# Kernel tuning notes

Hardware: AMD Instinct MI355X
Metric: run time of the kernel (lower is better)

## Reference

```python
import jax, jax.numpy as jnp
import numpy as np

B, S, H, KV, D, HID = 1, 2048, 32, 8, 128, 4096
SCALE = D ** -0.5
EPS = 1e-5
QMAX = 127.0  # 8-bit symmetric fake quant


def fake_quant(x):
    # per-tensor symmetric int8 fake quantization with straight-through estimator
    s = jnp.maximum(jnp.max(jnp.abs(x)), 1e-5) / QMAX
    q = jnp.clip(jnp.round(x / s), -QMAX - 1.0, QMAX) * s
    return x + jax.lax.stop_gradient(q - x)


def rms_norm(x, w):
    xf = x.astype(jnp.float32)
    var = jnp.mean(xf * xf, axis=-1, keepdims=True)
    return (xf * jax.lax.rsqrt(var + EPS)).astype(x.dtype) * w


def rotate_half(x):
    h = x.shape[-1] // 2
    return jnp.concatenate([-x[..., h:], x[..., :h]], axis=-1)


def qlinear(x, W):
    # QuantLinear: fake-quant activation and weight, then matmul (no bias)
    return fake_quant(x) @ fake_quant(W).T


def setup_inputs() -> dict:
    key = jax.random.key(0)
    ks = jax.random.split(key, 5)
    hidden_states = jax.random.normal(ks[0], (B, S, HID), jnp.float32)
    # RoPE tables
    inv_freq = 1.0 / (10000.0 ** (np.arange(0, D, 2, dtype=np.float32) / D))
    freqs = np.outer(np.arange(S, dtype=np.float32), inv_freq)  # [S, D/2]
    emb = np.concatenate([freqs, freqs], axis=-1)  # [S, D]
    cos = jnp.asarray(np.cos(emb))[None]  # [1,S,D]
    sin = jnp.asarray(np.sin(emb))[None]
    # causal additive mask [1,1,S,S]
    mask = jnp.where(np.tril(np.ones((S, S), dtype=bool)), 0.0, -1e9).astype(jnp.float32)[None, None]
    Wq = jax.random.normal(ks[1], (H * D, HID), jnp.float32) * 0.02
    Wk = jax.random.normal(ks[2], (KV * D, HID), jnp.float32) * 0.02
    Wv = jax.random.normal(ks[3], (KV * D, HID), jnp.float32) * 0.02
    Wo = jax.random.normal(ks[4], (HID, H * D), jnp.float32) * 0.02
    q_norm_w = jnp.ones((D,), jnp.float32)
    k_norm_w = jnp.ones((D,), jnp.float32)
    return dict(hidden_states=hidden_states, cos=cos, sin=sin, attention_mask=mask,
                Wq=Wq, Wk=Wk, Wv=Wv, Wo=Wo, q_norm_w=q_norm_w, k_norm_w=k_norm_w)


def reference(hidden_states, cos, sin, attention_mask, Wq, Wk, Wv, Wo, q_norm_w, k_norm_w):
    b, s, _ = hidden_states.shape
    q = qlinear(hidden_states, Wq).reshape(b, s, H, D).transpose(0, 2, 1, 3)   # [B,H,S,D]
    k = qlinear(hidden_states, Wk).reshape(b, s, KV, D).transpose(0, 2, 1, 3)  # [B,KV,S,D]
    v = qlinear(hidden_states, Wv).reshape(b, s, KV, D).transpose(0, 2, 1, 3)
    q = rms_norm(q, q_norm_w)
    k = rms_norm(k, k_norm_w)
    c = cos[:, None]  # unsqueeze head dim -> [1,1,S,D]
    sn = sin[:, None]
    q = q * c + rotate_half(q) * sn
    k = k * c + rotate_half(k) * sn
    n_rep = H // KV
    k = jnp.repeat(k, n_rep, axis=1)  # [B,H,S,D]
    v = jnp.repeat(v, n_rep, axis=1)
    # fake-quant around QK^T
    q = fake_quant(q)
    k = fake_quant(k)
    scores = jnp.einsum('bhqd,bhkd->bhqk', q, k) * SCALE + attention_mask
    p = jax.nn.softmax(scores.astype(jnp.float32), axis=-1).astype(q.dtype)
    # fake-quant around PV
    p = fake_quant(p)
    v = fake_quant(v)
    out = jnp.einsum('bhqk,bhkd->bhqd', p, v)
    out = out.transpose(0, 2, 1, 3).reshape(b, s, H * D)
    return qlinear(out, Wo)
```

## Files before the change

kernel.cpp:

```cpp
#include <hip/hip_runtime.h>
#include <hip/hip_bf16.h>
#include <math.h>
#include <stdint.h>

#define S_LEN 2048
#define NH    32
#define NKV   8
#define HD    128
#define HIDD  4096

typedef unsigned short u16;
typedef __attribute__((ext_vector_type(4))) int i32x4;

#define GLD16(g, l) __builtin_amdgcn_global_load_lds( \
    (const __attribute__((address_space(1))) void*)(g), \
    (__attribute__((address_space(3))) void*)(l), 16, 0, 0)


__device__ __forceinline__ float slot_scale(const unsigned* slot) {
    return fmaxf(__uint_as_float(*slot), 1e-5f) / 127.0f;
}

__device__ __forceinline__ float exp2_fast(float x) {
    float r; asm("v_exp_f32 %0, %1" : "=v"(r) : "v"(x)); return r;
}
__device__ __forceinline__ float log2_fast(float x) {
    float r; asm("v_log_f32 %0, %1" : "=v"(r) : "v"(x)); return r;
}

__device__ __forceinline__ int qint(float x, float s) {
    float q = rintf(x / s);
    q = fminf(fmaxf(q, -128.0f), 127.0f);
    return (int)q;
}

__device__ __forceinline__ void block_amax_atomic(float m, unsigned* slot) {
    __shared__ float wmax[8];
    const int lane = threadIdx.x & 63;
    const int wid  = threadIdx.x >> 6;
    const int nw   = blockDim.x >> 6;
    #pragma unroll
    for (int o = 32; o; o >>= 1) m = fmaxf(m, __shfl_xor(m, o));
    if (lane == 0) wmax[wid] = m;
    __syncthreads();
    if (threadIdx.x == 0) {
        float bm = wmax[0];
        for (int i = 1; i < nw; ++i) bm = fmaxf(bm, wmax[i]);
        atomicMax(slot, __float_as_uint(bm));
    }
}

struct Amax5Args { const float* p[5]; size_t n4[5]; };
__global__ __launch_bounds__(256) void absmax5_kernel(Amax5Args a, unsigned* slots) {
    const int t = blockIdx.y;
    const float4* x4 = (const float4*)a.p[t];
    const size_t n4 = a.n4[t];
    size_t i = (size_t)blockIdx.x * blockDim.x + threadIdx.x;
    size_t stride = (size_t)gridDim.x * blockDim.x;
    float m = 0.0f;
    for (; i < n4; i += stride) {
        float4 v = x4[i];
        m = fmaxf(m, fmaxf(fmaxf(fabsf(v.x), fabsf(v.y)), fmaxf(fabsf(v.z), fabsf(v.w))));
    }
    block_amax_atomic(m, slots + t);
}

struct Quant5Args { const float* p[5]; char* o[5]; size_t n4[5]; };
__global__ __launch_bounds__(256) void quant5_kernel(Quant5Args a, const unsigned* slots) {
    const int t = blockIdx.y;
    float s = slot_scale(slots + t);
    const float4* x4 = (const float4*)a.p[t];
    unsigned* o4 = (unsigned*)a.o[t];
    const size_t n4 = a.n4[t];
    size_t i = (size_t)blockIdx.x * blockDim.x + threadIdx.x;
    size_t stride = (size_t)gridDim.x * blockDim.x;
    for (; i < n4; i += stride) {
        float4 v = x4[i];
        unsigned o = (unsigned)(qint(v.x, s) & 255)
                   | ((unsigned)(qint(v.y, s) & 255) << 8)
                   | ((unsigned)(qint(v.z, s) & 255) << 16)
                   | ((unsigned)(qint(v.w, s) & 255) << 24);
        o4[i] = o;
    }
}

__global__ __launch_bounds__(256) void quant_kernel(const float* __restrict__ x,
                                                    size_t n4, const unsigned* slot,
                                                    char* __restrict__ out) {
    float s = slot_scale(slot);
    size_t i = (size_t)blockIdx.x * blockDim.x + threadIdx.x;
    size_t stride = (size_t)gridDim.x * blockDim.x;
    const float4* x4 = (const float4*)x;
    unsigned* o4 = (unsigned*)out;
    for (; i < n4; i += stride) {
        float4 v = x4[i];
        unsigned o = (unsigned)(qint(v.x, s) & 255)
                   | ((unsigned)(qint(v.y, s) & 255) << 8)
                   | ((unsigned)(qint(v.z, s) & 255) << 16)
                   | ((unsigned)(qint(v.w, s) & 255) << 24);
        o4[i] = o;
    }
}

__device__ __forceinline__ void gemm_body(const char* __restrict__ A,
                                          const char* __restrict__ B,
                                          float* __restrict__ C,
                                          int m0, int n0, int N, int K,
                                          float scale, unsigned* out_amax,
                                          char* Asm, char* Bsm) {
    const int tid  = threadIdx.x;
    const int lane = tid & 63;
    const int wave = tid >> 6;
    const int wr = (wave >> 1) * 64;
    const int wc = (wave & 1) * 64;
    const int l15 = lane & 15;
    const int l4  = lane >> 4;
    const int cx  = (l4 ^ (l15 & 3)) * 16;
    const int r0  = tid >> 2;
    const int sc  = ((tid & 3) ^ ((tid >> 2) & 3)) * 16;

    i32x4 acc[4][4];
    #pragma unroll
    for (int i = 0; i < 4; ++i)
        #pragma unroll
        for (int j = 0; j < 4; ++j) acc[i][j] = (i32x4){0, 0, 0, 0};

    auto STAGE = [&](int buf, int k0) {
        GLD16(&A[(size_t)(m0 + r0) * K + k0 + sc],      &Asm[buf * 8192 + wave * 1024]);
        GLD16(&A[(size_t)(m0 + 64 + r0) * K + k0 + sc], &Asm[buf * 8192 + 4096 + wave * 1024]);
        GLD16(&B[(size_t)(n0 + r0) * K + k0 + sc],      &Bsm[buf * 8192 + wave * 1024]);
        GLD16(&B[(size_t)(n0 + 64 + r0) * K + k0 + sc], &Bsm[buf * 8192 + 4096 + wave * 1024]);
    };

    const int NT = K >> 6;
    STAGE(0, 0);
    STAGE(1, 64);
    int cur = 0;
    for (int t = 0; t < NT; ++t) {
        if (t + 1 < NT) {
            asm volatile("s_waitcnt vmcnt(4)" ::: "memory");
        } else {
            asm volatile("s_waitcnt vmcnt(0)" ::: "memory");
        }
        __builtin_amdgcn_sched_barrier(0);
        __builtin_amdgcn_s_barrier();
        __builtin_amdgcn_sched_barrier(0);
        if (t + 2 < NT) {
            int nb = cur + 2; if (nb >= 3) nb -= 3;
            STAGE(nb, (t + 2) << 6);
        }
        i32x4 af[4], bfr[4];
        #pragma unroll
        for (int i = 0; i < 4; ++i)
            af[i] = *(const i32x4*)&Asm[cur * 8192 + (wr + i * 16 + l15) * 64 + cx];
        #pragma unroll
        for (int j = 0; j < 4; ++j)
            bfr[j] = *(const i32x4*)&Bsm[cur * 8192 + (wc + j * 16 + l15) * 64 + cx];
        #pragma unroll
        for (int i = 0; i < 4; ++i)
            #pragma unroll
            for (int j = 0; j < 4; ++j)
                acc[i][j] = __builtin_amdgcn_mfma_i32_16x16x64_i8(af[i], bfr[j], acc[i][j], 0, 0, 0);
        cur += 1; if (cur == 3) cur = 0;
    }

    float lm = 0.0f;
    #pragma unroll
    for (int i = 0; i < 4; ++i)
        #pragma unroll
        for (int j = 0; j < 4; ++j)
            #pragma unroll
            for (int r = 0; r < 4; ++r) {
                int row = m0 + wr + i * 16 + l4 * 4 + r;
                int col = n0 + wc + j * 16 + l15;
                float v = (float)acc[i][j][r] * scale;
                C[(size_t)row * N + col] = v;
                lm = fmaxf(lm, fabsf(v));
            }
    __syncthreads();
    if (out_amax) block_amax_atomic(lm, out_amax);
}

__global__ __launch_bounds__(256) void gemm_qkv_kernel(const char* __restrict__ Aq,
                                                       const char* __restrict__ Wqq,
                                                       const char* __restrict__ Wkq,
                                                       const char* __restrict__ Wvq,
                                                       float* __restrict__ qf,
                                                       float* __restrict__ kf,
                                                       float* __restrict__ vf,
                                                       const unsigned* __restrict__ slots,
                                                       unsigned* v_amax) {
    __shared__ __align__(16) char Asm[3 * 8192];
    __shared__ __align__(16) char Bsm[3 * 8192];
    int bid = blockIdx.x;
    int swz = (bid & 7) * 96 + (bid >> 3);
    int x = swz & 15, y = swz >> 4;
    const char* B; float* C; int N, nb; const unsigned* sB; unsigned* am = nullptr;
    if (y < 32)      { B = Wqq; C = qf; N = NH * HD;  nb = y;      sB = slots + 1; }
    else if (y < 40) { B = Wkq; C = kf; N = NKV * HD; nb = y - 32; sB = slots + 2; }
    else             { B = Wvq; C = vf; N = NKV * HD; nb = y - 40; sB = slots + 3; am = v_amax; }
    float scale = slot_scale(slots + 0) * slot_scale(sB);
    gemm_body(Aq, B, C, x * 128, nb * 128, N, HIDD, scale, am, Asm, Bsm);
}

__global__ __launch_bounds__(256) void gemm_o_kernel(const char* __restrict__ A,
                                                     const char* __restrict__ Woq,
                                                     float* __restrict__ C,
                                                     const unsigned* __restrict__ slots) {
    __shared__ __align__(16) char Asm[3 * 8192];
    __shared__ __align__(16) char Bsm[3 * 8192];
    int bid = blockIdx.x;
    int swz = (bid & 7) * 64 + (bid >> 3);
    int x = swz & 15, y = swz >> 4;
    float scale = slot_scale(slots + 8) * slot_scale(slots + 4);
    gemm_body(A, Woq, C, x * 128, y * 128, NH * HD, HIDD, scale, nullptr, Asm, Bsm);
}

__global__ __launch_bounds__(256) void rmsrope2_kernel(float* __restrict__ qx,
                                                       float* __restrict__ kx,
                                                       const float* __restrict__ cosb,
                                                       const float* __restrict__ sinb,
                                                       const float* __restrict__ qw,
                                                       const float* __restrict__ kw,
                                                       unsigned* slots) {
    const int which = blockIdx.y;
    float* x = which ? kx : qx;
    const float* w = which ? kw : qw;
    const int s_shift = which ? 3 : 5;
    const int nrows = which ? (S_LEN * NKV) : (S_LEN * NH);
    unsigned* slot = slots + (which ? 6 : 5);

    const int lane = threadIdx.x & 63;
    const int wid  = threadIdx.x >> 6;
    const float wa = w[lane];
    const float wb = w[lane + 64];
    float lm = 0.0f;
    for (int row = blockIdx.x * 4 + wid; row < nrows; row += gridDim.x * 4) {
        int s = row >> s_shift;
        float* xr = x + (size_t)row * 128;
        float a = xr[lane], b = xr[lane + 64];
        float ss = a * a + b * b;
        #pragma unroll
        for (int o = 32; o; o >>= 1) ss += __shfl_xor(ss, o);
        float inv = 1.0f / sqrtf(ss * (1.0f / 128.0f) + 1e-5f);
        float ya = (a * inv) * wa;
        float yb = (b * inv) * wb;
        const float* cr = cosb + (size_t)s * 128;
        const float* sr = sinb + (size_t)s * 128;
        float o0 = ya * cr[lane]      - yb * sr[lane];
        float o1 = yb * cr[lane + 64] + ya * sr[lane + 64];
        xr[lane] = o0;
        xr[lane + 64] = o1;
        lm = fmaxf(lm, fmaxf(fabsf(o0), fabsf(o1)));
    }
    block_amax_atomic(lm, slot);
}

__global__ __launch_bounds__(256) void quant_qk2_kernel(const float* __restrict__ qx,
                                                        const float* __restrict__ kx,
                                                        const unsigned* slots,
                                                        char* __restrict__ qq,
                                                        char* __restrict__ kq) {
    int tid = blockIdx.x * 256 + threadIdx.x;
    const int qtot = S_LEN * NH * HD;
    if (tid < qtot) {
        float s = slot_scale(slots + 5);
        int d  = tid & 127;
        int h  = (tid >> 7) & 31;
        int sp = tid >> 12;
        qq[((size_t)h * S_LEN + sp) * 128 + d] = (char)qint(qx[tid], s);
    } else {
        tid -= qtot;
        float s = slot_scale(slots + 6);
        int d  = tid & 127;
        int h  = (tid >> 7) & 7;
        int sp = tid >> 10;
        kq[((size_t)h * S_LEN + sp) * 128 + d] = (char)qint(kx[tid], s);
    }
}

__global__ __launch_bounds__(256) void quant_v_kernel(const float* __restrict__ x,
                                                      const unsigned* slot,
                                                      char* __restrict__ out) {
    __shared__ unsigned char t8[64][36];
    const float s = slot_scale(slot);
    const int t   = threadIdx.x;
    const int sp0 = blockIdx.x * 64;
    const int d0  = blockIdx.y * 32;
    const int kvh = blockIdx.z;
    const int dl = t & 31;
    const int sb = t >> 5;
    #pragma unroll
    for (int j = 0; j < 8; ++j) {
        int spl = sb + j * 8;
        float v = x[((size_t)(sp0 + spl) * NKV + kvh) * 128 + d0 + dl];
        t8[spl][dl] = (unsigned char)qint(v, s);
    }
    __syncthreads();
    const int dd = t >> 3;
    const int ch = t & 7;
    unsigned lo = 0, hi = 0;
    #pragma unroll
    for (int j = 0; j < 4; ++j) lo |= (unsigned)t8[ch * 8 + j][dd] << (8 * j);
    #pragma unroll
    for (int j = 0; j < 4; ++j) hi |= (unsigned)t8[ch * 8 + 4 + j][dd] << (8 * j);
    *(uint2*)&out[((size_t)kvh * 128 + d0 + dd) * S_LEN + sp0 + ch * 8] = make_uint2(lo, hi);
}

__global__ __launch_bounds__(256) void attn_kernel(const char* __restrict__ Qq,
                                                   const char* __restrict__ Kq,
                                                   const char* __restrict__ Vt,
                                                   const unsigned* sq_slot,
                                                   const unsigned* sk_slot,
                                                   const unsigned* sv_slot,
                                                   float* __restrict__ O,
                                                   unsigned* amax_slot) {
    __shared__ __align__(16) char Klds[64 * 144];
    __shared__ __align__(16) char Vlds[128 * 80];
    __shared__ __align__(16) char pldsB[4][16 * 80];
    __shared__ __align__(16) char pldsS[4][16 * 80];

    const int tid  = threadIdx.x;
    const int lane = tid & 63;
    const int wave = tid >> 6;
    const int h  = blockIdx.y;
    const int kv = h >> 2;
    const int l15 = lane & 15;
    const int l4  = lane >> 4;
    const size_t kvS = (size_t)kv * S_LEN;

    const int qtS = blockIdx.x;
    const int qtB = 31 - qtS;
    const int qr0S = qtS * 64 + wave * 16;
    const int qr0B = qtB * 64 + wave * 16;

    const float sq = slot_scale(sq_slot);
    const float sk = slot_scale(sk_slot);
    const float sv = slot_scale(sv_slot);
    const float qs2 = sq * sk * 0.08838834764831845f * 1.4426950408889634f;
    const float osc = (1.0f / 127.0f) * sv;
    const float NEG = -1e30f;

    i32x4 qfS[2], qfB[2];
    {
        const char* qpS = Qq + ((size_t)h * S_LEN + qr0S + l15) * 128 + l4 * 16;
        const char* qpB = Qq + ((size_t)h * S_LEN + qr0B + l15) * 128 + l4 * 16;
        qfS[0] = *(const i32x4*)(qpS); qfS[1] = *(const i32x4*)(qpS + 64);
        qfB[0] = *(const i32x4*)(qpB); qfB[1] = *(const i32x4*)(qpB + 64);
    }

    auto qk_block = [&](int hb, const i32x4* qf2) -> i32x4 {
        i32x4 sacc = {0, 0, 0, 0};
        #pragma unroll
        for (int c = 0; c < 2; ++c) {
            i32x4 kfa = *(const i32x4*)&Klds[(hb * 16 + l15) * 144 + c * 64 + l4 * 16];
            sacc = __builtin_amdgcn_mfma_i32_16x16x64_i8(kfa, qf2[c], sacc, 0, 0, 0);
        }
        return sacc;
    };

    float mS = NEG, lS = 0.0f, mB = NEG, lB = 0.0f;

    auto p1_interior = [&](int hb, const i32x4* qf2, float& m_l, float& l_l) {
        i32x4 sacc = qk_block(hb, qf2);
        float x0 = (float)sacc[0] * qs2, x1 = (float)sacc[1] * qs2;
        float x2 = (float)sacc[2] * qs2, x3 = (float)sacc[3] * qs2;
        float bm = fmaxf(fmaxf(x0, x1), fmaxf(x2, x3));
        float mn = fmaxf(m_l, bm);
        float ps = exp2_fast(x0 - mn) + exp2_fast(x1 - mn)
                 + exp2_fast(x2 - mn) + exp2_fast(x3 - mn);
        l_l = l_l * exp2_fast(m_l - mn) + ps;
        m_l = mn;
    };
    auto p1_diag = [&](int hb, const i32x4* qf2, float& m_l, float& l_l) {
        i32x4 sacc = qk_block(hb, qf2);
        float x[4];
        #pragma unroll
        for (int r = 0; r < 4; ++r) {
            float v = (float)sacc[r] * qs2;
            x[r] = ((l4 * 4 + r) > l15) ? NEG : v;
        }
        float bm = fmaxf(fmaxf(x[0], x[1]), fmaxf(x[2], x[3]));
        float mn = fmaxf(m_l, bm);
        float ps = exp2_fast(x[0] - mn) + exp2_fast(x[1] - mn)
                 + exp2_fast(x[2] - mn) + exp2_fast(x[3] - mn);
        l_l = l_l * exp2_fast(m_l - mn) + ps;
        m_l = mn;
    };

    i32x4 kreg[2];
    #pragma unroll
    for (int c = 0; c < 2; ++c) {
        int idx = c * 256 + tid;
        kreg[c] = *(const i32x4*)&Kq[(kvS + (idx >> 3)) * 128 + (idx & 7) * 16];
    }
    #pragma unroll 1
    for (int kc = 0; kc <= qtB; ++kc) {
        __syncthreads();
        #pragma unroll
        for (int c = 0; c < 2; ++c) {
            int idx = c * 256 + tid;
            *(i32x4*)&Klds[(idx >> 3) * 144 + (idx & 7) * 16] = kreg[c];
        }
        __syncthreads();
        if (kc < qtB) {
            #pragma unroll
            for (int c = 0; c < 2; ++c) {
                int idx = c * 256 + tid;
                kreg[c] = *(const i32x4*)&Kq[(kvS + (kc + 1) * 64 + (idx >> 3)) * 128 + (idx & 7) * 16];
            }
        }
        if (kc < qtB) {
            p1_interior(0, qfB, mB, lB); p1_interior(1, qfB, mB, lB);
            p1_interior(2, qfB, mB, lB); p1_interior(3, qfB, mB, lB);
        } else {
            #pragma unroll
            for (int hb = 0; hb < 4; ++hb) {
                if (hb < wave) p1_interior(hb, qfB, mB, lB);
                else if (hb == wave) p1_diag(hb, qfB, mB, lB);
            }
        }
        if (kc < qtS) {
            p1_interior(0, qfS, mS, lS); p1_interior(1, qfS, mS, lS);
            p1_interior(2, qfS, mS, lS); p1_interior(3, qfS, mS, lS);
        } else if (kc == qtS) {
            #pragma unroll
            for (int hb = 0; hb < 4; ++hb) {
                if (hb < wave) p1_interior(hb, qfS, mS, lS);
                else if (hb == wave) p1_diag(hb, qfS, mS, lS);
            }
        }
    }
    auto merge = [&](float m_l, float l_l) -> float {
        float m2 = fmaxf(m_l, __shfl_xor(m_l, 16));
        float mfin = fmaxf(m2, __shfl_xor(m2, 32));
        float t = l_l * exp2_fast(m_l - mfin);
        t += __shfl_xor(t, 16);
        t += __shfl_xor(t, 32);
        return mfin - log2_fast(127.0f / t);
    };
    const float cS = merge(mS, lS);
    const float cB = merge(mB, lB);

    i32x4 oaccS[8], oaccB[8];
    #pragma unroll
    for (int dt = 0; dt < 8; ++dt) {
        oaccS[dt] = (i32x4){0, 0, 0, 0};
        oaccB[dt] = (i32x4){0, 0, 0, 0};
    }

    auto p2_interior = [&](int hb, const i32x4* qf2, float c) -> unsigned {
        i32x4 sacc = qk_block(hb, qf2);
        unsigned pack = 0;
        #pragma unroll
        for (int r = 0; r < 4; ++r) {
            float pq = rintf(exp2_fast(fmaf((float)sacc[r], qs2, -c)));
            pack |= ((unsigned)(int)pq) << (8 * r);
        }
        return pack;
    };
    auto p2_diag = [&](int hb, const i32x4* qf2, float c) -> unsigned {
        i32x4 sacc = qk_block(hb, qf2);
        unsigned pack = 0;
        #pragma unroll
        for (int r = 0; r < 4; ++r) {
            float p = exp2_fast(fmaf((float)sacc[r], qs2, -c));
            float pq = ((l4 * 4 + r) > l15) ? 0.0f : rintf(p);
            pack |= ((unsigned)(int)pq) << (8 * r);
        }
        return pack;
    };
    auto pv8 = [&](char (*plds)[16 * 80], i32x4* oacc) {
        i32x4 pf = *(const i32x4*)&plds[wave][l15 * 80 + l4 * 16];
        __builtin_amdgcn_s_setprio(1);
        #pragma unroll
        for (int dt = 0; dt < 8; ++dt) {
            i32x4 vfb = *(const i32x4*)&Vlds[(dt * 16 + l15) * 80 + l4 * 16];
            oacc[dt] = __builtin_amdgcn_mfma_i32_16x16x64_i8(pf, vfb, oacc[dt], 0, 0, 0);
        }
        __builtin_amdgcn_s_setprio(0);
    };

    i32x4 vreg[2];
    #pragma unroll
    for (int c = 0; c < 2; ++c) {
        int idx = c * 256 + tid;
        kreg[c] = *(const i32x4*)&Kq[(kvS + (idx >> 3)) * 128 + (idx & 7) * 16];
        vreg[c] = *(const i32x4*)&Vt[((size_t)kv * 128 + (idx >> 2)) * S_LEN + (idx & 3) * 16];
    }
    #pragma unroll 1
    for (int kc = 0; kc <= qtB; ++kc) {
        __syncthreads();
        #pragma unroll
        for (int c = 0; c < 2; ++c) {
            int idx = c * 256 + tid;
            *(i32x4*)&Klds[(idx >> 3) * 144 + (idx & 7) * 16] = kreg[c];
            *(i32x4*)&Vlds[(idx >> 2) * 80 + (idx & 3) * 16] = vreg[c];
        }
        __syncthreads();
        if (kc < qtB) {
            #pragma unroll
            for (int c = 0; c < 2; ++c) {
                int idx = c * 256 + tid;
                kreg[c] = *(const i32x4*)&Kq[(kvS + (kc + 1) * 64 + (idx >> 3)) * 128 + (idx & 7) * 16];
                vreg[c] = *(const i32x4*)&Vt[((size_t)kv * 128 + (idx >> 2)) * S_LEN + (kc + 1) * 64 + (idx & 3) * 16];
            }
        }
        if (kc < qtB) {
            #pragma unroll
            for (int hb = 0; hb < 4; ++hb)
                *(unsigned*)&pldsB[wave][l15 * 80 + hb * 16 + l4 * 4] = p2_interior(hb, qfB, cB);
        } else {
            #pragma unroll
            for (int hb = 0; hb < 4; ++hb) {
                unsigned pack = 0;
                if (hb < wave) pack = p2_interior(hb, qfB, cB);
                else if (hb == wave) pack = p2_diag(hb, qfB, cB);
                *(unsigned*)&pldsB[wave][l15 * 80 + hb * 16 + l4 * 4] = pack;
            }
        }
        pv8(pldsB, oaccB);
        if (kc < qtS) {
            #pragma unroll
            for (int hb = 0; hb < 4; ++hb)
                *(unsigned*)&pldsS[wave][l15 * 80 + hb * 16 + l4 * 4] = p2_interior(hb, qfS, cS);
            pv8(pldsS, oaccS);
        } else if (kc == qtS) {
            #pragma unroll
            for (int hb = 0; hb < 4; ++hb) {
                unsigned pack = 0;
                if (hb < wave) pack = p2_interior(hb, qfS, cS);
                else if (hb == wave) pack = p2_diag(hb, qfS, cS);
                *(unsigned*)&pldsS[wave][l15 * 80 + hb * 16 + l4 * 4] = pack;
            }
            pv8(pldsS, oaccS);
        }
    }

    float lm = 0.0f;
    #pragma unroll
    for (int dt = 0; dt < 8; ++dt)
        #pragma unroll
        for (int r = 0; r < 4; ++r) {
            float vB = (float)oaccB[dt][r] * osc;
            float vS = (float)oaccS[dt][r] * osc;
            int col = h * 128 + dt * 16 + l15;
            O[(size_t)(qr0B + l4 * 4 + r) * (NH * 128) + col] = vB;
            O[(size_t)(qr0S + l4 * 4 + r) * (NH * 128) + col] = vS;
            lm = fmaxf(lm, fmaxf(fabsf(vB), fabsf(vS)));
        }
    block_amax_atomic(lm, amax_slot);
}

extern "C" void kernel_launch(void* const* d_in, const int* in_sizes, int n_in,
                              void* d_out, int out_size, void* d_ws, size_t ws_size,
                              hipStream_t stream) {
    const float* hs   = (const float*)d_in[0];
    const float* cosb = (const float*)d_in[1];
    const float* sinb = (const float*)d_in[2];
    const float* Wq   = (const float*)d_in[4];
    const float* Wk   = (const float*)d_in[5];
    const float* Wv   = (const float*)d_in[6];
    const float* Wo   = (const float*)d_in[7];
    const float* qnw  = (const float*)d_in[8];
    const float* knw  = (const float*)d_in[9];
    float* out = (float*)d_out;

    char* ws = (char*)d_ws;
    unsigned* slots = (unsigned*)ws;
    size_t off = 256;
    auto take = [&](size_t bytes) { size_t o = off; off += (bytes + 255) & ~(size_t)255; return o; };
    char*  hsq  = (char*)(ws + take((size_t)S_LEN * HIDD));
    char*  Wqq  = (char*)(ws + take((size_t)NH * HD * HIDD));
    char*  Wkq  = (char*)(ws + take((size_t)NKV * HD * HIDD));
    char*  Wvq  = (char*)(ws + take((size_t)NKV * HD * HIDD));
    char*  Woq  = (char*)(ws + take((size_t)HIDD * NH * HD));
    float* qf   = (float*)(ws + take((size_t)S_LEN * NH * HD * 4));
    float* kf   = (float*)(ws + take((size_t)S_LEN * NKV * HD * 4));
    float* vf   = (float*)(ws + take((size_t)S_LEN * NKV * HD * 4));
    char*  qq   = (char*)(ws + take((size_t)NH * S_LEN * HD));
    char*  kq   = (char*)(ws + take((size_t)NKV * S_LEN * HD));
    char*  vtq  = (char*)(ws + take((size_t)NKV * HD * S_LEN));
    float* attnf = qf;
    char*  attnq = hsq;

    hipMemsetAsync(ws, 0, 64, stream);

    const size_t n_hs = (size_t)S_LEN * HIDD;
    const size_t n_wq = (size_t)NH * HD * HIDD;
    const size_t n_wk = (size_t)NKV * HD * HIDD;

    Amax5Args aa;
    aa.p[0] = hs; aa.p[1] = Wq; aa.p[2] = Wk; aa.p[3] = Wv; aa.p[4] = Wo;
    aa.n4[0] = n_hs / 4; aa.n4[1] = n_wq / 4; aa.n4[2] = n_wk / 4;
    aa.n4[3] = n_wk / 4; aa.n4[4] = n_wq / 4;
    absmax5_kernel<<<dim3(512, 5), 256, 0, stream>>>(aa, slots);

    Quant5Args qa;
    qa.p[0] = hs; qa.p[1] = Wq; qa.p[2] = Wk; qa.p[3] = Wv; qa.p[4] = Wo;
    qa.o[0] = hsq; qa.o[1] = Wqq; qa.o[2] = Wkq; qa.o[3] = Wvq; qa.o[4] = Woq;
    qa.n4[0] = n_hs / 4; qa.n4[1] = n_wq / 4; qa.n4[2] = n_wk / 4;
    qa.n4[3] = n_wk / 4; qa.n4[4] = n_wq / 4;
    quant5_kernel<<<dim3(1024, 5), 256, 0, stream>>>(qa, slots);

    gemm_qkv_kernel<<<768, 256, 0, stream>>>(hsq, Wqq, Wkq, Wvq, qf, kf, vf,
                                             slots, slots + 7);

    rmsrope2_kernel<<<dim3(1024, 2), 256, 0, stream>>>(qf, kf, cosb, sinb, qnw, knw, slots);

    quant_qk2_kernel<<<40960, 256, 0, stream>>>(qf, kf, slots, qq, kq);
    quant_v_kernel<<<dim3(32, 4, 8), 256, 0, stream>>>(vf, slots + 7, vtq);

    attn_kernel<<<dim3(16, NH), 256, 0, stream>>>(qq, kq, vtq,
                                                  slots + 5, slots + 6, slots + 7,
                                                  attnf, slots + 8);

    quant_kernel<<<2048, 256, 0, stream>>>(attnf, n_hs / 4, slots + 8, attnq);
    gemm_o_kernel<<<512, 256, 0, stream>>>(attnq, Woq, out, slots);
    (void)in_sizes; (void)n_in; (void)out_size; (void)ws_size;
}
```

Baseline: 355.2 us.

## Switch int8 GEMM to K=128 tiles with double buffering and wider LDS swizzle

The shared int8 GEMM body moves from a triple-buffered K=64 pipeline with manual vmcnt waits to a double-buffered K=128 pipeline. Each tile is processed as two MFMA sub-steps, and the LDS layout uses an 8-way XOR swizzle over 128-byte rows. The intent is to halve the number of barrier iterations and amortise sync overhead across more MFMA work per stage. In exchange it drops the explicit waitcnt control, relies on __syncthreads to drain loads, and uses more LDS per block (64KB), which may lower occupancy or overlap.

```diff
diff --git a/kernel.cpp b/kernel.cpp
--- a/kernel.cpp
+++ b/kernel.cpp
@@ -115,9 +115,8 @@
     const int wc = (wave & 1) * 64;
     const int l15 = lane & 15;
     const int l4  = lane >> 4;
-    const int cx  = (l4 ^ (l15 & 3)) * 16;
-    const int r0  = tid >> 2;
-    const int sc  = ((tid & 3) ^ ((tid >> 2) & 3)) * 16;
+    const int cx0 = ((l4)     ^ (l15 & 7)) * 16;
+    const int cx1 = ((l4 + 4) ^ (l15 & 7)) * 16;
 
     i32x4 acc[4][4];
     #pragma unroll
@@ -126,42 +125,42 @@
         for (int j = 0; j < 4; ++j) acc[i][j] = (i32x4){0, 0, 0, 0};
 
     auto STAGE = [&](int buf, int k0) {
-        GLD16(&A[(size_t)(m0 + r0) * K + k0 + sc],      &Asm[buf * 8192 + wave * 1024]);
-        GLD16(&A[(size_t)(m0 + 64 + r0) * K + k0 + sc], &Asm[buf * 8192 + 4096 + wave * 1024]);
-        GLD16(&B[(size_t)(n0 + r0) * K + k0 + sc],      &Bsm[buf * 8192 + wave * 1024]);
-        GLD16(&B[(size_t)(n0 + 64 + r0) * K + k0 + sc], &Bsm[buf * 8192 + 4096 + wave * 1024]);
-    };
-
-    const int NT = K >> 6;
+        #pragma unroll
+        for (int i = 0; i < 4; ++i) {
+            int chunk = i * 256 + tid;
+            int row = chunk >> 3;
+            int sc  = ((chunk & 7) ^ (row & 7)) * 16;
+            GLD16(&A[(size_t)(m0 + row) * K + k0 + sc],
+                  &Asm[buf * 16384 + (i * 256 + wave * 64) * 16]);
+            GLD16(&B[(size_t)(n0 + row) * K + k0 + sc],
+                  &Bsm[buf * 16384 + (i * 256 + wave * 64) * 16]);
+        }
+    };
+
+    const int NT = K >> 7;
     STAGE(0, 0);
-    STAGE(1, 64);
+    __syncthreads();
     int cur = 0;
     for (int t = 0; t < NT; ++t) {
-        if (t + 1 < NT) {
-            asm volatile("s_waitcnt vmcnt(4)" ::: "memory");
-        } else {
-            asm volatile("s_waitcnt vmcnt(0)" ::: "memory");
-        }
-        __builtin_amdgcn_sched_barrier(0);
-        __builtin_amdgcn_s_barrier();
-        __builtin_amdgcn_sched_barrier(0);
-        if (t + 2 < NT) {
-            int nb = cur + 2; if (nb >= 3) nb -= 3;
-            STAGE(nb, (t + 2) << 6);
-        }
-        i32x4 af[4], bfr[4];
-        #pragma unroll
-        for (int i = 0; i < 4; ++i)
-            af[i] = *(const i32x4*)&Asm[cur * 8192 + (wr + i * 16 + l15) * 64 + cx];
-        #pragma unroll
-        for (int j = 0; j < 4; ++j)
-            bfr[j] = *(const i32x4*)&Bsm[cur * 8192 + (wc + j * 16 + l15) * 64 + cx];
-        #pragma unroll
-        for (int i = 0; i < 4; ++i)
+        if (t + 1 < NT) STAGE(cur ^ 1, (t + 1) << 7);
+        #pragma unroll
+        for (int kk = 0; kk < 2; ++kk) {
+            const int cx = kk ? cx1 : cx0;
+            i32x4 af[4], bfr[4];
+            #pragma unroll
+            for (int i = 0; i < 4; ++i)
+                af[i] = *(const i32x4*)&Asm[cur * 16384 + (wr + i * 16 + l15) * 128 + cx];
             #pragma unroll
             for (int j = 0; j < 4; ++j)
-                acc[i][j] = __builtin_amdgcn_mfma_i32_16x16x64_i8(af[i], bfr[j], acc[i][j], 0, 0, 0);
-        cur += 1; if (cur == 3) cur = 0;
+                bfr[j] = *(const i32x4*)&Bsm[cur * 16384 + (wc + j * 16 + l15) * 128 + cx];
+            #pragma unroll
+            for (int i = 0; i < 4; ++i)
+                #pragma unroll
+                for (int j = 0; j < 4; ++j)
+                    acc[i][j] = __builtin_amdgcn_mfma_i32_16x16x64_i8(af[i], bfr[j], acc[i][j], 0, 0, 0);
+        }
+        __syncthreads();
+        cur ^= 1;
     }
 
     float lm = 0.0f;
@@ -177,7 +176,6 @@
                 C[(size_t)row * N + col] = v;
                 lm = fmaxf(lm, fabsf(v));
             }
-    __syncthreads();
     if (out_amax) block_amax_atomic(lm, out_amax);
 }
 
@@ -190,8 +188,8 @@
                                                        float* __restrict__ vf,
                                                        const unsigned* __restrict__ slots,
                                                        unsigned* v_amax) {
-    __shared__ __align__(16) char Asm[3 * 8192];
-    __shared__ __align__(16) char Bsm[3 * 8192];
+    __shared__ __align__(16) char Asm[2 * 16384];
+    __shared__ __align__(16) char Bsm[2 * 16384];
     int bid = blockIdx.x;
     int swz = (bid & 7) * 96 + (bid >> 3);
     int x = swz & 15, y = swz >> 4;
@@ -207,8 +205,8 @@
                                                      const char* __restrict__ Woq,
                                                      float* __restrict__ C,
                                                      const unsigned* __restrict__ slots) {
-    __shared__ __align__(16) char Asm[3 * 8192];
-    __shared__ __align__(16) char Bsm[3 * 8192];
+    __shared__ __align__(16) char Asm[2 * 16384];
+    __shared__ __align__(16) char Bsm[2 * 16384];
     int bid = blockIdx.x;
     int swz = (bid & 7) * 64 + (bid >> 3);
     int x = swz & 15, y = swz >> 4;
```

Measured after the change: 367.2 us. 1.03x slower.
